# Kernel optimization log

Measured on AMD Instinct MI355X. Metric: run time of the kernel, lower is better.

The kernel has to match this reference:

```python
import jax, jax.numpy as jnp
import numpy as np

N = 50000
DEG = 16
E = N * DEG
IN_F, HID, OUT_F = 512, 128, 64
SLOPE = 0.2


def setup_inputs() -> dict:
    key = jax.random.key(0)
    ks = jax.random.split(key, 10)
    row_ptr = jnp.arange(N + 1, dtype=jnp.int64) * DEG          # uniform-degree CSR
    col_idx = jax.random.randint(ks[0], (E,), 0, N, dtype=jnp.int64)
    x = jax.random.normal(ks[1], (N, IN_F), dtype=jnp.float32)
    s1 = 1.0 / np.sqrt(IN_F)
    s2 = 1.0 / np.sqrt(HID)
    return {
        "row_ptr": row_ptr,
        "col_idx": col_idx,
        "input_feature": x,
        "W1": jax.random.normal(ks[2], (IN_F, HID), dtype=jnp.float32) * s1,
        "attn_l1": jax.random.normal(ks[3], (HID,), dtype=jnp.float32) * s2,
        "attn_r1": jax.random.normal(ks[4], (HID,), dtype=jnp.float32) * s2,
        "bias1": jnp.zeros((HID,), dtype=jnp.float32),
        "W2": jax.random.normal(ks[5], (HID, OUT_F), dtype=jnp.float32) * s2,
        "attn_l2": jax.random.normal(ks[6], (OUT_F,), dtype=jnp.float32) * 0.125,
        "attn_r2": jax.random.normal(ks[7], (OUT_F,), dtype=jnp.float32) * 0.125,
        "bias2": jnp.zeros((OUT_F,), dtype=jnp.float32),
    }


def gat_layer(row_ptr, col_idx, x, W, attn_l, attn_r, bias):
    n = row_ptr.shape[0] - 1
    e = col_idx.shape[0]
    h = x @ W                                   # [N, F] dense GEMM
    el = h @ attn_l                             # [N] dst attention term
    er = h @ attn_r                             # [N] src attention term
    # edge -> destination row via CSR row_ptr
    dst = jnp.searchsorted(row_ptr, jnp.arange(e, dtype=row_ptr.dtype), side="right") - 1
    src = col_idx
    score = jax.nn.leaky_relu(el[dst] + er[src], negative_slope=SLOPE)  # [E]
    # neighborhood softmax over edges sharing a destination
    smax = jax.ops.segment_max(score, dst, num_segments=n)
    ex = jnp.exp(score - smax[dst])
    ssum = jax.ops.segment_sum(ex, dst, num_segments=n)
    alpha = ex / ssum[dst]                      # [E]
    # weighted gather-scatter aggregation
    out = jax.ops.segment_sum(alpha[:, None] * h[src], dst, num_segments=n)
    return out + bias


def reference(row_ptr, col_idx, input_feature, W1, attn_l1, attn_r1, bias1,
              W2, attn_l2, attn_r2, bias2):
    x = gat_layer(row_ptr, col_idx, input_feature, W1, attn_l1, attn_r1, bias1)
    x = gat_layer(row_ptr, col_idx, x, W2, attn_l2, attn_r2, bias2)
    return x
```

## Files before the change

### kernel.cpp

```cpp
#include <hip/hip_runtime.h>
#include <hip/hip_bf16.h>

#define Nn 50000
#define DEG 16
#define IN_F 512
#define HID 128
#define OUT_F 64
#define SLOPE 0.2f

typedef __attribute__((ext_vector_type(8))) short bf16x8;
typedef __attribute__((ext_vector_type(4))) float f32x4;
typedef __attribute__((ext_vector_type(4))) unsigned int u32x4;

__device__ __forceinline__ unsigned short f2bf(float f) {
    return __builtin_bit_cast(unsigned short, __float2bfloat16(f));
}
__device__ __forceinline__ float bf2f(unsigned short u) {
    return __bfloat162float(__builtin_bit_cast(__hip_bfloat16, u));
}
__device__ __forceinline__ void async_copy16(const void* g, void* l) {
    __builtin_amdgcn_global_load_lds(
        (const __attribute__((address_space(1))) unsigned int*)g,
        (__attribute__((address_space(3))) unsigned int*)l, 16, 0, 0);
}

__global__ void __launch_bounds__(256) prep_kernel(
        const float* __restrict__ W1, const float* __restrict__ W2,
        const float* __restrict__ al1, const float* __restrict__ ar1,
        const float* __restrict__ b1, const int* __restrict__ row_ptr,
        unsigned short* __restrict__ w12c, float* __restrict__ uv,
        float* __restrict__ c2v, int* __restrict__ flag64) {
    const int tid = threadIdx.x;
    const int lane = tid & 63;
    const int w = tid >> 6;
    const int k = blockIdx.x * 4 + w;
    if (blockIdx.x == 0 && tid == 0) {
        *flag64 = (row_ptr[1] == DEG) ? 0 : 1;
    }
    const float* w1row = W1 + (size_t)k * HID;

    float acc = 0.f;
    #pragma unroll 8
    for (int j = 0; j < HID; ++j)
        acc += w1row[j] * W2[j * OUT_F + lane];
    {
        int ch = k >> 7, kin = k & 127;
        int bsrc = kin >> 3, j = kin & 7;
        int bdst = bsrc ^ (lane & 7);
        w12c[ch * 8192 + lane * 128 + bdst * 8 + j] = f2bf(acc);
    }

    float pu = w1row[lane] * al1[lane] + w1row[lane + 64] * al1[lane + 64];
    float pv = w1row[lane] * ar1[lane] + w1row[lane + 64] * ar1[lane + 64];
    #pragma unroll
    for (int m = 1; m < 64; m <<= 1) {
        pu += __shfl_xor(pu, m);
        pv += __shfl_xor(pv, m);
    }
    if (lane == 0) { uv[k] = pu; uv[IN_F + k] = pv; }

    if (blockIdx.x == 0 && w == 0) {
        float cacc = 0.f;
        #pragma unroll 8
        for (int j = 0; j < HID; ++j) cacc += b1[j] * W2[j * OUT_F + lane];
        c2v[lane] = cacc;
    }
}

template<int K>
__global__ void __launch_bounds__(256) gemm1_tiled(
        const float* __restrict__ Af, const unsigned short* __restrict__ w12c,
        const float* __restrict__ uv,
        unsigned short* __restrict__ G, float* __restrict__ el,
        float* __restrict__ er, int M) {
    constexpr int NCH = K / 128;
    __shared__ float As[64 * 128];
    __shared__ unsigned short Bs[64 * 128];

    const int tid  = threadIdx.x;
    const int lane = tid & 63;
    const int w    = tid >> 6;
    const int ln   = lane & 15, q = lane >> 4;
    const int r2   = lane >> 5, b = lane & 31;
    const int mb   = blockIdx.x * 64;

    f32x4 acc[4] = {};
    float sl = 0.f, sr = 0.f;

    for (int ch = 0; ch < NCH; ++ch) {
        const char* gb = (const char*)w12c + ch * 16384;
        #pragma unroll
        for (int i = 0; i < 4; ++i) {
            int slot = w * 4 + i;
            async_copy16(gb + slot * 1024 + lane * 16, (char*)Bs + slot * 1024);
        }
        #pragma unroll
        for (int i = 0; i < 8; ++i) {
            int rl = w * 16 + i * 2 + r2;
            int rg = mb + rl; if (rg > M - 1) rg = M - 1;
            int c  = rl & 7;
            const float* src = Af + (size_t)rg * K + ch * 128 + ((b ^ c) << 2);
            async_copy16(src, (char*)As + (size_t)(w * 16 + i * 2) * 512);
        }
        __syncthreads();

        const float* up = uv + ch * 128;
        const float* vp = uv + K + ch * 128;
        const int c = ln & 7;
        #pragma unroll
        for (int ks = 0; ks < 4; ++ks) {
            const int b0 = ks * 8 + q * 2;
            f32x4 a0 = *(const f32x4*)&As[(w * 16 + ln) * 128 + ((b0 ^ c) << 2)];
            f32x4 a1 = *(const f32x4*)&As[(w * 16 + ln) * 128 + (((b0 + 1) ^ c) << 2)];
            f32x4 u0 = *(const f32x4*)(up + ks * 32 + q * 8);
            f32x4 u1 = *(const f32x4*)(up + ks * 32 + q * 8 + 4);
            f32x4 v0 = *(const f32x4*)(vp + ks * 32 + q * 8);
            f32x4 v1 = *(const f32x4*)(vp + ks * 32 + q * 8 + 4);
            bf16x8 af;
            #pragma unroll
            for (int jj = 0; jj < 4; ++jj) {
                af[jj]     = (short)f2bf(a0[jj]);
                af[jj + 4] = (short)f2bf(a1[jj]);
                sl += a0[jj] * u0[jj] + a1[jj] * u1[jj];
                sr += a0[jj] * v0[jj] + a1[jj] * v1[jj];
            }
            #pragma unroll
            for (int nt = 0; nt < 4; ++nt) {
                const int bb = ks * 4 + q;
                bf16x8 bfr = *(const bf16x8*)&Bs[(nt * 16 + ln) * 128 + ((bb ^ c) << 3)];
                acc[nt] = __builtin_amdgcn_mfma_f32_16x16x32_bf16(af, bfr, acc[nt], 0, 0, 0);
            }
        }
        __syncthreads();
    }

    sl += __shfl_xor(sl, 16); sl += __shfl_xor(sl, 32);
    sr += __shfl_xor(sr, 16); sr += __shfl_xor(sr, 32);
    const int rowe = mb + w * 16 + ln;
    if (q == 0 && rowe < M) { el[rowe] = sl; er[rowe] = sr; }

    #pragma unroll
    for (int r = 0; r < 4; ++r) {
        int grow = mb + w * 16 + q * 4 + r;
        if (grow < M) {
            #pragma unroll
            for (int nt = 0; nt < 4; ++nt)
                G[(size_t)grow * OUT_F + nt * 16 + ln] = f2bf(acc[nt][r]);
        }
    }
}

template<int MODE>
__global__ void __launch_bounds__(256) agg_k(
        const int* __restrict__ col, const int* __restrict__ flag64,
        const float* __restrict__ el, const float* __restrict__ er,
        const unsigned short* __restrict__ Hs, const float* __restrict__ addv,
        const float* __restrict__ alv, const float* __restrict__ arv,
        unsigned short* __restrict__ Ho, float* __restrict__ elo,
        float* __restrict__ ero, float* __restrict__ Fo) {
    const int tid  = threadIdx.x;
    const int lane = tid & 63;
    const int w    = tid >> 6;
    const int ln   = lane & 15, q = lane >> 4;
    const int g16  = w * 4 + q;
    const int nA   = blockIdx.x * 32 + g16 * 2;
    const int nB   = nA + 1;
    const int nAc  = nA < Nn ? nA : Nn - 1;
    const int nBc  = nB < Nn ? nB : Nn - 1;
    const int use64 = *flag64;

    int eA = nAc * DEG + ln, eB = nBc * DEG + ln;
    int srcA = use64 ? (int)((const long long*)col)[eA] : col[eA];
    int srcB = use64 ? (int)((const long long*)col)[eB] : col[eB];
    float scA = el[nAc] + er[srcA];
    float scB = el[nBc] + er[srcB];
    scA = scA >= 0.f ? scA : SLOPE * scA;
    scB = scB >= 0.f ? scB : SLOPE * scB;
    float mxA = scA, mxB = scB;
    #pragma unroll
    for (int m = 1; m < 16; m <<= 1) {
        mxA = fmaxf(mxA, __shfl_xor(mxA, m, 16));
        mxB = fmaxf(mxB, __shfl_xor(mxB, m, 16));
    }
    float exA = __expf(scA - mxA), exB = __expf(scB - mxB);
    float smA = exA, smB = exB;
    #pragma unroll
    for (int m = 1; m < 16; m <<= 1) {
        smA += __shfl_xor(smA, m, 16);
        smB += __shfl_xor(smB, m, 16);
    }
    float alA = exA / smA, alB = exB / smB;

    const int half = ln >> 3, cc = ln & 7;
    bf16x8 hA[8], hB[8];
    #pragma unroll
    for (int p = 0; p < 8; ++p) {
        int sjA = __shfl(srcA, p * 2 + half, 16);
        int sjB = __shfl(srcB, p * 2 + half, 16);
        hA[p] = *(const bf16x8*)&Hs[(size_t)sjA * OUT_F + cc * 8];
        hB[p] = *(const bf16x8*)&Hs[(size_t)sjB * OUT_F + cc * 8];
    }
    float aA[8] = {}, aB[8] = {};
    #pragma unroll
    for (int p = 0; p < 8; ++p) {
        float wA = __shfl(alA, p * 2 + half, 16);
        float wB = __shfl(alB, p * 2 + half, 16);
        #pragma unroll
        for (int c = 0; c < 8; ++c) {
            aA[c] += wA * bf2f((unsigned short)hA[p][c]);
            aB[c] += wB * bf2f((unsigned short)hB[p][c]);
        }
    }
    #pragma unroll
    for (int c = 0; c < 8; ++c) {
        aA[c] += __shfl_xor(aA[c], 8, 16);
        aB[c] += __shfl_xor(aB[c], 8, 16);
        float ad = addv[cc * 8 + c];
        aA[c] += ad;
        aB[c] += ad;
    }

    if (MODE == 0) {
        float plA = 0.f, prA = 0.f, plB = 0.f, prB = 0.f;
        #pragma unroll
        for (int c = 0; c < 8; ++c) {
            float av = alv[cc * 8 + c], bv = arv[cc * 8 + c];
            plA += aA[c] * av;  prA += aA[c] * bv;
            plB += aB[c] * av;  prB += aB[c] * bv;
        }
        #pragma unroll
        for (int m = 1; m < 8; m <<= 1) {
            plA += __shfl_xor(plA, m, 16);  prA += __shfl_xor(prA, m, 16);
            plB += __shfl_xor(plB, m, 16);  prB += __shfl_xor(prB, m, 16);
        }
        if (ln == 0) {
            if (nA < Nn) { elo[nA] = plA; ero[nA] = prA; }
            if (nB < Nn) { elo[nB] = plB; ero[nB] = prB; }
        }
        if (half == 0) {
            unsigned int pkA[4], pkB[4];
            #pragma unroll
            for (int c = 0; c < 4; ++c) {
                pkA[c] = (unsigned int)f2bf(aA[2 * c]) |
                         ((unsigned int)f2bf(aA[2 * c + 1]) << 16);
                pkB[c] = (unsigned int)f2bf(aB[2 * c]) |
                         ((unsigned int)f2bf(aB[2 * c + 1]) << 16);
            }
            if (nA < Nn) *(u32x4*)&Ho[(size_t)nA * OUT_F + cc * 8] = *(u32x4*)pkA;
            if (nB < Nn) *(u32x4*)&Ho[(size_t)nB * OUT_F + cc * 8] = *(u32x4*)pkB;
        }
    } else {
        if (half == 0) {
            f32x4 oA0, oA1, oB0, oB1;
            #pragma unroll
            for (int c = 0; c < 4; ++c) {
                oA0[c] = aA[c]; oA1[c] = aA[c + 4];
                oB0[c] = aB[c]; oB1[c] = aB[c + 4];
            }
            if (nA < Nn) {
                *(f32x4*)&Fo[(size_t)nA * OUT_F + cc * 8]     = oA0;
                *(f32x4*)&Fo[(size_t)nA * OUT_F + cc * 8 + 4] = oA1;
            }
            if (nB < Nn) {
                *(f32x4*)&Fo[(size_t)nB * OUT_F + cc * 8]     = oB0;
                *(f32x4*)&Fo[(size_t)nB * OUT_F + cc * 8 + 4] = oB1;
            }
        }
    }
}

extern "C" void kernel_launch(void* const* d_in, const int* in_sizes, int n_in,
                              void* d_out, int out_size, void* d_ws, size_t ws_size,
                              hipStream_t stream) {
    const int*   row_ptr = (const int*)d_in[0];
    const int*   col_idx = (const int*)d_in[1];
    const float* x   = (const float*)d_in[2];
    const float* W1  = (const float*)d_in[3];
    const float* al1 = (const float*)d_in[4];
    const float* ar1 = (const float*)d_in[5];
    const float* b1  = (const float*)d_in[6];
    const float* W2  = (const float*)d_in[7];
    const float* al2 = (const float*)d_in[8];
    const float* ar2 = (const float*)d_in[9];
    const float* b2  = (const float*)d_in[10];
    float* out = (float*)d_out;

    float* ws = (float*)d_ws;
    unsigned short* g   = (unsigned short*)ws;
    unsigned short* h2b = (unsigned short*)(ws + 1600000);
    float* el1 = ws + 3200000;
    float* er1 = ws + 3250000;
    float* el2 = ws + 3300000;
    float* er2 = ws + 3350000;
    unsigned short* w12c = (unsigned short*)(ws + 3400000);
    float* uv  = ws + 3420000;
    float* c2v = ws + 3421024;
    int* flag64 = (int*)(ws + 3421100);

    prep_kernel<<<128, 256, 0, stream>>>(
        W1, W2, al1, ar1, b1, row_ptr, w12c, uv, c2v, flag64);

    gemm1_tiled<IN_F><<<(Nn + 63) / 64, 256, 0, stream>>>(
        x, w12c, uv, g, el1, er1, Nn);

    agg_k<0><<<(Nn + 31) / 32, 256, 0, stream>>>(
        col_idx, flag64, el1, er1, g, c2v, al2, ar2, h2b, el2, er2, nullptr);

    agg_k<1><<<(Nn + 31) / 32, 256, 0, stream>>>(
        col_idx, flag64, el2, er2, h2b, b2, nullptr, nullptr,
        nullptr, nullptr, nullptr, out);
}
```

Measured before the change: 222.3 us.

## Split aggregation feature dimension into two halves for L2-resident gathers

Result: slower. 240.9 us (+8.4%).

```diff
diff --git a/kernel.cpp b/kernel.cpp
--- a/kernel.cpp
+++ b/kernel.cpp
@@ -71,8 +71,8 @@
 __global__ void __launch_bounds__(256) gemm1_tiled(
         const float* __restrict__ Af, const unsigned short* __restrict__ w12c,
         const float* __restrict__ uv,
-        unsigned short* __restrict__ G, float* __restrict__ el,
-        float* __restrict__ er, int M) {
+        unsigned short* __restrict__ G0, unsigned short* __restrict__ G1,
+        float* __restrict__ el, float* __restrict__ er, int M) {
     constexpr int NCH = K / 128;
     __shared__ float As[64 * 128];
     __shared__ unsigned short Bs[64 * 128];
@@ -144,18 +144,21 @@
         int grow = mb + w * 16 + q * 4 + r;
         if (grow < M) {
             #pragma unroll
-            for (int nt = 0; nt < 4; ++nt)
-                G[(size_t)grow * OUT_F + nt * 16 + ln] = f2bf(acc[nt][r]);
-        }
-    }
-}
-
-template<int MODE>
-__global__ void __launch_bounds__(256) agg_k(
+            for (int nt = 0; nt < 4; ++nt) {
+                unsigned short* T = (nt < 2) ? G0 : G1;
+                T[(size_t)grow * 32 + (nt & 1) * 16 + ln] = f2bf(acc[nt][r]);
+            }
+        }
+    }
+}
+
+template<int MODE, int HALF>
+__global__ void __launch_bounds__(256) agg_half(
         const int* __restrict__ col, const int* __restrict__ flag64,
         const float* __restrict__ el, const float* __restrict__ er,
         const unsigned short* __restrict__ Hs, const float* __restrict__ addv,
         const float* __restrict__ alv, const float* __restrict__ arv,
+        float* __restrict__ alpha,
         unsigned short* __restrict__ Ho, float* __restrict__ elo,
         float* __restrict__ ero, float* __restrict__ Fo) {
     const int tid  = threadIdx.x;
@@ -172,39 +175,48 @@
     int eA = nAc * DEG + ln, eB = nBc * DEG + ln;
     int srcA = use64 ? (int)((const long long*)col)[eA] : col[eA];
     int srcB = use64 ? (int)((const long long*)col)[eB] : col[eB];
-    float scA = el[nAc] + er[srcA];
-    float scB = el[nBc] + er[srcB];
-    scA = scA >= 0.f ? scA : SLOPE * scA;
-    scB = scB >= 0.f ? scB : SLOPE * scB;
-    float mxA = scA, mxB = scB;
-    #pragma unroll
-    for (int m = 1; m < 16; m <<= 1) {
-        mxA = fmaxf(mxA, __shfl_xor(mxA, m, 16));
-        mxB = fmaxf(mxB, __shfl_xor(mxB, m, 16));
-    }
-    float exA = __expf(scA - mxA), exB = __expf(scB - mxB);
-    float smA = exA, smB = exB;
-    #pragma unroll
-    for (int m = 1; m < 16; m <<= 1) {
-        smA += __shfl_xor(smA, m, 16);
-        smB += __shfl_xor(smB, m, 16);
-    }
-    float alA = exA / smA, alB = exB / smB;
-
-    const int half = ln >> 3, cc = ln & 7;
-    bf16x8 hA[8], hB[8];
-    #pragma unroll
-    for (int p = 0; p < 8; ++p) {
-        int sjA = __shfl(srcA, p * 2 + half, 16);
-        int sjB = __shfl(srcB, p * 2 + half, 16);
-        hA[p] = *(const bf16x8*)&Hs[(size_t)sjA * OUT_F + cc * 8];
-        hB[p] = *(const bf16x8*)&Hs[(size_t)sjB * OUT_F + cc * 8];
+
+    float alA, alB;
+    if (HALF == 0) {
+        float scA = el[nAc] + er[srcA];
+        float scB = el[nBc] + er[srcB];
+        scA = scA >= 0.f ? scA : SLOPE * scA;
+        scB = scB >= 0.f ? scB : SLOPE * scB;
+        float mxA = scA, mxB = scB;
+        #pragma unroll
+        for (int m = 1; m < 16; m <<= 1) {
+            mxA = fmaxf(mxA, __shfl_xor(mxA, m, 16));
+            mxB = fmaxf(mxB, __shfl_xor(mxB, m, 16));
+        }
+        float exA = __expf(scA - mxA), exB = __expf(scB - mxB);
+        float smA = exA, smB = exB;
+        #pragma unroll
+        for (int m = 1; m < 16; m <<= 1) {
+            smA += __shfl_xor(smA, m, 16);
+            smB += __shfl_xor(smB, m, 16);
+        }
+        alA = exA / smA;  alB = exB / smB;
+        if (nA < Nn) alpha[eA] = alA;
+        if (nB < Nn) alpha[eB] = alB;
+    } else {
+        alA = alpha[eA];
+        alB = alpha[eB];
+    }
+
+    const int es = ln >> 2, cc = ln & 3;
+    bf16x8 hA[4], hB[4];
+    #pragma unroll
+    for (int p = 0; p < 4; ++p) {
+        int sjA = __shfl(srcA, p * 4 + es, 16);
+        int sjB = __shfl(srcB, p * 4 + es, 16);
+        hA[p] = *(const bf16x8*)&Hs[(size_t)sjA * 32 + cc * 8];
+        hB[p] = *(const bf16x8*)&Hs[(size_t)sjB * 32 + cc * 8];
     }
     float aA[8] = {}, aB[8] = {};
     #pragma unroll
-    for (int p = 0; p < 8; ++p) {
-        float wA = __shfl(alA, p * 2 + half, 16);
-        float wB = __shfl(alB, p * 2 + half, 16);
+    for (int p = 0; p < 4; ++p) {
+        float wA = __shfl(alA, p * 4 + es, 16);
+        float wB = __shfl(alB, p * 4 + es, 16);
         #pragma unroll
         for (int c = 0; c < 8; ++c) {
             aA[c] += wA * bf2f((unsigned short)hA[p][c]);
@@ -213,9 +225,11 @@
     }
     #pragma unroll
     for (int c = 0; c < 8; ++c) {
+        aA[c] += __shfl_xor(aA[c], 4, 16);
         aA[c] += __shfl_xor(aA[c], 8, 16);
+        aB[c] += __shfl_xor(aB[c], 4, 16);
         aB[c] += __shfl_xor(aB[c], 8, 16);
-        float ad = addv[cc * 8 + c];
+        float ad = addv[HALF * 32 + cc * 8 + c];
         aA[c] += ad;
         aB[c] += ad;
     }
@@ -224,20 +238,25 @@
         float plA = 0.f, prA = 0.f, plB = 0.f, prB = 0.f;
         #pragma unroll
         for (int c = 0; c < 8; ++c) {
-            float av = alv[cc * 8 + c], bv = arv[cc * 8 + c];
+            float av = alv[HALF * 32 + cc * 8 + c];
+            float bv = arv[HALF * 32 + cc * 8 + c];
             plA += aA[c] * av;  prA += aA[c] * bv;
             plB += aB[c] * av;  prB += aB[c] * bv;
         }
-        #pragma unroll
-        for (int m = 1; m < 8; m <<= 1) {
-            plA += __shfl_xor(plA, m, 16);  prA += __shfl_xor(prA, m, 16);
-            plB += __shfl_xor(plB, m, 16);  prB += __shfl_xor(prB, m, 16);
-        }
+        plA += __shfl_xor(plA, 1, 16); plA += __shfl_xor(plA, 2, 16);
+        prA += __shfl_xor(prA, 1, 16); prA += __shfl_xor(prA, 2, 16);
+        plB += __shfl_xor(plB, 1, 16); plB += __shfl_xor(plB, 2, 16);
+        prB += __shfl_xor(prB, 1, 16); prB += __shfl_xor(prB, 2, 16);
         if (ln == 0) {
-            if (nA < Nn) { elo[nA] = plA; ero[nA] = prA; }
-            if (nB < Nn) { elo[nB] = plB; ero[nB] = prB; }
-        }
-        if (half == 0) {
+            if (HALF == 0) {
+                if (nA < Nn) { elo[nA] = plA; ero[nA] = prA; }
+                if (nB < Nn) { elo[nB] = plB; ero[nB] = prB; }
+            } else {
+                if (nA < Nn) { elo[nA] += plA; ero[nA] += prA; }
+                if (nB < Nn) { elo[nB] += plB; ero[nB] += prB; }
+            }
+        }
+        if (es == 0) {
             unsigned int pkA[4], pkB[4];
             #pragma unroll
             for (int c = 0; c < 4; ++c) {
@@ -246,11 +265,11 @@
                 pkB[c] = (unsigned int)f2bf(aB[2 * c]) |
                          ((unsigned int)f2bf(aB[2 * c + 1]) << 16);
             }
-            if (nA < Nn) *(u32x4*)&Ho[(size_t)nA * OUT_F + cc * 8] = *(u32x4*)pkA;
-            if (nB < Nn) *(u32x4*)&Ho[(size_t)nB * OUT_F + cc * 8] = *(u32x4*)pkB;
+            if (nA < Nn) *(u32x4*)&Ho[(size_t)nA * 32 + cc * 8] = *(u32x4*)pkA;
+            if (nB < Nn) *(u32x4*)&Ho[(size_t)nB * 32 + cc * 8] = *(u32x4*)pkB;
         }
     } else {
-        if (half == 0) {
+        if (es == 0) {
             f32x4 oA0, oA1, oB0, oB1;
             #pragma unroll
             for (int c = 0; c < 4; ++c) {
@@ -258,12 +277,12 @@
                 oB0[c] = aB[c]; oB1[c] = aB[c + 4];
             }
             if (nA < Nn) {
-                *(f32x4*)&Fo[(size_t)nA * OUT_F + cc * 8]     = oA0;
-                *(f32x4*)&Fo[(size_t)nA * OUT_F + cc * 8 + 4] = oA1;
+                *(f32x4*)&Fo[(size_t)nA * OUT_F + HALF * 32 + cc * 8]     = oA0;
+                *(f32x4*)&Fo[(size_t)nA * OUT_F + HALF * 32 + cc * 8 + 4] = oA1;
             }
             if (nB < Nn) {
-                *(f32x4*)&Fo[(size_t)nB * OUT_F + cc * 8]     = oB0;
-                *(f32x4*)&Fo[(size_t)nB * OUT_F + cc * 8 + 4] = oB1;
+                *(f32x4*)&Fo[(size_t)nB * OUT_F + HALF * 32 + cc * 8]     = oB0;
+                *(f32x4*)&Fo[(size_t)nB * OUT_F + HALF * 32 + cc * 8 + 4] = oB1;
             }
         }
     }
@@ -286,27 +305,38 @@
     float* out = (float*)d_out;
 
     float* ws = (float*)d_ws;
-    unsigned short* g   = (unsigned short*)ws;
-    unsigned short* h2b = (unsigned short*)(ws + 1600000);
+    unsigned short* g0   = (unsigned short*)ws;
+    unsigned short* g1   = (unsigned short*)(ws + 800000);
+    unsigned short* h2b0 = (unsigned short*)(ws + 1600000);
+    unsigned short* h2b1 = (unsigned short*)(ws + 2400000);
     float* el1 = ws + 3200000;
     float* er1 = ws + 3250000;
     float* el2 = ws + 3300000;
     float* er2 = ws + 3350000;
-    unsigned short* w12c = (unsigned short*)(ws + 3400000);
-    float* uv  = ws + 3420000;
-    float* c2v = ws + 3421024;
-    int* flag64 = (int*)(ws + 3421100);
+    float* alpha1 = ws + 3400000;
+    float* alpha2 = ws + 4200000;
+    unsigned short* w12c = (unsigned short*)(ws + 5000000);
+    float* uv  = ws + 5020000;
+    float* c2v = ws + 5021100;
+    int* flag64 = (int*)(ws + 5021200);
 
     prep_kernel<<<128, 256, 0, stream>>>(
         W1, W2, al1, ar1, b1, row_ptr, w12c, uv, c2v, flag64);
 
     gemm1_tiled<IN_F><<<(Nn + 63) / 64, 256, 0, stream>>>(
-        x, w12c, uv, g, el1, er1, Nn);
-
-    agg_k<0><<<(Nn + 31) / 32, 256, 0, stream>>>(
-        col_idx, flag64, el1, er1, g, c2v, al2, ar2, h2b, el2, er2, nullptr);
-
-    agg_k<1><<<(Nn + 31) / 32, 256, 0, stream>>>(
-        col_idx, flag64, el2, er2, h2b, b2, nullptr, nullptr,
+        x, w12c, uv, g0, g1, el1, er1, Nn);
+
+    agg_half<0, 0><<<(Nn + 31) / 32, 256, 0, stream>>>(
+        col_idx, flag64, el1, er1, g0, c2v, al2, ar2, alpha1,
+        h2b0, el2, er2, nullptr);
+    agg_half<0, 1><<<(Nn + 31) / 32, 256, 0, stream>>>(
+        col_idx, flag64, el1, er1, g1, c2v, al2, ar2, alpha1,
+        h2b1, el2, er2, nullptr);
+
+    agg_half<1, 0><<<(Nn + 31) / 32, 256, 0, stream>>>(
+        col_idx, flag64, el2, er2, h2b0, b2, nullptr, nullptr, alpha2,
         nullptr, nullptr, nullptr, out);
-}
+    agg_half<1, 1><<<(Nn + 31) / 32, 256, 0, stream>>>(
+        col_idx, flag64, el2, er2, h2b1, b2, nullptr, nullptr, alpha2,
+        nullptr, nullptr, nullptr, out);
+}
```
